# Performance work log

Measured on AMD Instinct MI355X. Metric: run time of the kernel, lower is better.

## Reference

```python
import jax, jax.numpy as jnp
import numpy as np

B, N, R = 2, 64, 16
D = 64      # node_dim_in
H = 256     # hidden_dim
EOUT = 64   # edge_dim_out
PSTEP = 2


def _lin_init(key, fi, fo):
    k1, k2 = jax.random.split(key)
    s = 1.0 / np.sqrt(fi)
    W = jax.random.uniform(k1, (fi, fo), minval=-s, maxval=s, dtype=jnp.float32)
    b = jax.random.uniform(k2, (fo,), minval=-s, maxval=s, dtype=jnp.float32)
    return W, b


def setup_inputs() -> dict:
    key = jax.random.key(0)
    ks = jax.random.split(key, 11)
    node_rep = jax.random.normal(ks[0], (B, N, R, D), dtype=jnp.float32)
    ne_W, ne_b = _lin_init(ks[1], D, H)          # node_encoder
    ee_W, ee_b = _lin_init(ks[2], 2 * D, H)      # edge_encoder (edge_rep is None)
    np_W1, np_b1 = _lin_init(ks[3], 3 * H, H)    # node_propagator
    np_W2, np_b2 = _lin_init(ks[4], H, H)
    ep0_W1, ep0_b1 = _lin_init(ks[5], 3 * H, H)  # edge_propagators[0]
    ep0_W2, ep0_b2 = _lin_init(ks[6], H, H)
    ep1_W1, ep1_b1 = _lin_init(ks[7], 3 * H, H)  # edge_propagators[1]
    ep1_W2, ep1_b2 = _lin_init(ks[8], H, H)
    pr_W1, pr_b1 = _lin_init(ks[9], 2 * H, H)    # edge_predictor
    pr_W2, pr_b2 = _lin_init(ks[10], H, EOUT)
    return dict(node_rep=node_rep, ne_W=ne_W, ne_b=ne_b, ee_W=ee_W, ee_b=ee_b,
                np_W1=np_W1, np_b1=np_b1, np_W2=np_W2, np_b2=np_b2,
                ep0_W1=ep0_W1, ep0_b1=ep0_b1, ep0_W2=ep0_W2, ep0_b2=ep0_b2,
                ep1_W1=ep1_W1, ep1_b1=ep1_b1, ep1_W2=ep1_W2, ep1_b2=ep1_b2,
                pr_W1=pr_W1, pr_b1=pr_b1, pr_W2=pr_W2, pr_b2=pr_b2)


def _propnet(node_rep, ne_W, ne_b, ee_W, ee_b, np_W1, np_b1, np_W2, np_b2,
             ep_params, pr_W1, pr_b1, pr_W2, pr_b2):
    relu = jax.nn.relu
    # node encoder: [B,N,R,H]
    node_enc = relu(node_rep @ ne_W + ne_b)
    # edge encoder on cat(node_rep_r, node_rep_s): split the weight instead of
    # materializing the [B,N,N,R,2D] repeated-concat tensor (same math).
    # receiver varies over axis 1, sender over axis 2.
    edge_enc = relu(node_rep[:, :, None] @ ee_W[:D]
                    + node_rep[:, None, :] @ ee_W[D:] + ee_b)  # [B,N,N,R,H]
    node_effect = node_enc
    edge_effect = edge_enc
    for (W1, b1, W2, b2) in ep_params:
        # edge propagator on cat(effect_r, effect_s, edge_effect)
        h = relu(node_effect[:, :, None] @ W1[:H]
                 + node_effect[:, None, :] @ W1[H:2 * H]
                 + edge_effect @ W1[2 * H:] + b1)
        edge_effect = relu(h @ W2 + b2)                 # [B,N,N,R,H]
        agg = edge_effect.sum(axis=2)                   # sum over senders -> [B,N,R,H]
        g = relu(node_enc @ np_W1[:H]
                 + node_effect @ np_W1[H:2 * H]
                 + agg @ np_W1[2 * H:] + np_b1)
        node_effect = relu(g @ np_W2 + np_b2)
    # edge predictor on cat(edge_effect, edge_enc) -> split weight
    p = relu(edge_effect @ pr_W1[:H] + edge_enc @ pr_W1[H:] + pr_b1)
    edge_pred = p @ pr_W2 + pr_b2                       # [B,N,N,R,EOUT]
    return edge_pred


def reference(node_rep, ne_W, ne_b, ee_W, ee_b, np_W1, np_b1, np_W2, np_b2,
              ep0_W1, ep0_b1, ep0_W2, ep0_b2, ep1_W1, ep1_b1, ep1_W2, ep1_b2,
              pr_W1, pr_b1, pr_W2, pr_b2):
    ep_params = [(ep0_W1, ep0_b1, ep0_W2, ep0_b2), (ep1_W1, ep1_b1, ep1_W2, ep1_b2)]
    return _propnet(node_rep, ne_W, ne_b, ee_W, ee_b, np_W1, np_b1, np_W2, np_b2,
                    ep_params, pr_W1, pr_b1, pr_W2, pr_b2)
```

## Files before the change

### kernel.cpp

```cpp
#include <hip/hip_runtime.h>
#include <hip/hip_bf16.h>


typedef __attribute__((ext_vector_type(8))) short short8;
typedef __attribute__((ext_vector_type(4))) float f32x4;
typedef __attribute__((ext_vector_type(2))) unsigned int u32x2;

#define DI __device__ __forceinline__

constexpr size_t WF_SZ = 131072;
constexpr size_t OFF_NEW  = 14 * WF_SZ;
constexpr size_t OFF_EE1  = OFF_NEW + 32768;
constexpr size_t OFF_EE2  = OFF_EE1 + 32768;
constexpr size_t OFF_PW2  = OFF_EE2 + 32768;
constexpr size_t OFF_NENC = OFF_PW2 + 32768;
constexpr size_t OFF_X1   = OFF_NENC + (size_t)2048 * 256 * 2;
constexpr size_t SM = (size_t)2048 * 256 * 4;
constexpr size_t OFF_X2  = OFF_X1 + SM;
constexpr size_t OFF_E1  = OFF_X2 + SM;
constexpr size_t OFF_E2  = OFF_E1 + SM;
constexpr size_t OFF_NE1 = OFF_E2 + SM;
constexpr size_t OFF_AGG = OFF_NE1 + SM;
constexpr size_t OFF_IMG = OFF_AGG + 2 * SM;

DI unsigned short f2bf(float f) {
    unsigned u = __builtin_bit_cast(unsigned, f);
    u += 0x7fffu + ((u >> 16) & 1u);
    return (unsigned short)(u >> 16);
}

DI int kmap(int g, int e) { return 4 * g + (e & 3) + ((e >> 2) << 4); }

DI void dma16(const void* g, void* l) {
    __builtin_amdgcn_global_load_lds((const __attribute__((address_space(1))) void*)g,
                                     (__attribute__((address_space(3))) void*)l, 16, 0, 0);
}

__global__ __launch_bounds__(64) void kconv(const float* ep0W1, const float* ep0W2,
                                            const float* ep1W1, const float* ep1W2,
                                            const float* prW1, const float* prW2,
                                            const float* npW1, const float* npW2,
                                            const float* neW, const float* eeW,
                                            unsigned short* wsu)
{
    int bid = blockIdx.x, l = threadIdx.x;
    const float* src; unsigned short* dst; int NT = 16, ld = 256, f;
    if (bid < 1792) {
        int m = bid >> 7; f = bid & 127;
        switch (m) {
            case 0:  src = ep0W1 + 512 * 256; break;
            case 1:  src = ep0W2;             break;
            case 2:  src = ep1W1 + 512 * 256; break;
            case 3:  src = ep1W2;             break;
            case 4:  src = prW1;              break;
            case 5:  src = prW1 + 256 * 256;  break;
            case 6:  src = ep0W1;             break;
            case 7:  src = ep0W1 + 256 * 256; break;
            case 8:  src = npW1 + 256 * 256;  break;
            case 9:  src = npW1 + 512 * 256;  break;
            case 10: src = npW1;              break;
            case 11: src = npW2;              break;
            case 12: src = ep1W1;             break;
            default: src = ep1W1 + 256 * 256; break;
        }
        dst = wsu + (size_t)m * (WF_SZ / 2);
    } else if (bid < 1888) {
        int m = (bid - 1792) >> 5; f = (bid - 1792) & 31;
        src = (m == 0) ? neW : (m == 1) ? eeW : eeW + 64 * 256;
        dst = wsu + ((m == 0) ? OFF_NEW : (m == 1) ? OFF_EE1 : OFF_EE2) / 2;
    } else {
        f = bid - 1888; NT = 4; ld = 64; src = prW2; dst = wsu + OFF_PW2 / 2;
    }
    int kt = f / NT, nt = f % NT;
    int g = l >> 4, c = nt * 16 + (l & 15);
    unsigned short* o = dst + (size_t)((kt * NT + nt) * 64 + l) * 8;
#pragma unroll
    for (int e = 0; e < 8; ++e) {
        int k = 32 * kt + kmap(g, e);
        o[e] = f2bf(src[(size_t)k * ld + c]);
    }
}

template <int LDB>
DI short8 load_afrag(const unsigned char* lds, int row, int kt, int g) {
    int sw = (row & 7) << 4;
    int kb = 64 * kt + 8 * g;
    union { short8 s; u32x2 u[2]; } u_;
    u_.u[0] = *(const u32x2*)(lds + row * LDB + (kb ^ sw));
    u_.u[1] = *(const u32x2*)(lds + row * LDB + ((kb + 32) ^ sw));
    return u_.s;
}

template <int MI>
DI void zero_acc(f32x4 (&acc)[MI][4]) {
#pragma unroll
    for (int mi = 0; mi < MI; ++mi)
#pragma unroll
        for (int ni = 0; ni < 4; ++ni) acc[mi][ni] = (f32x4){0.f, 0.f, 0.f, 0.f};
}

template <int MI, int KT, int LDB>
DI void gemm_tile(const unsigned char* lds, const unsigned short* Wf,
                  f32x4 (&acc)[MI][4], int wv, int l) {
    const int g = l >> 4, l15 = l & 15;
    for (int kt = 0; kt < KT; ++kt) {
        short8 af[MI];
#pragma unroll
        for (int mi = 0; mi < MI; ++mi) af[mi] = load_afrag<LDB>(lds, 16 * mi + l15, kt, g);
        short8 bf[4];
#pragma unroll
        for (int ni = 0; ni < 4; ++ni)
            bf[ni] = *(const short8*)(Wf + (size_t)((kt * 16 + 4 * wv + ni) * 64 + l) * 8);
#pragma unroll
        for (int ni = 0; ni < 4; ++ni)
#pragma unroll
            for (int mi = 0; mi < MI; ++mi)
                acc[mi][ni] = __builtin_amdgcn_mfma_f32_16x16x32_bf16(af[mi], bf[ni], acc[mi][ni], 0, 0, 0);
    }
}

DI void store_tile_f32(float* dst, int r0, f32x4 (&acc)[4][4], int wv, int l) {
    int g = l >> 4, l15 = l & 15;
#pragma unroll
    for (int ni = 0; ni < 4; ++ni) {
        int col = 64 * wv + 16 * ni + l15;
#pragma unroll
        for (int mi = 0; mi < 4; ++mi)
#pragma unroll
            for (int q = 0; q < 4; ++q)
                dst[(size_t)(r0 + 16 * mi + 4 * g + q) * 256 + col] = acc[mi][ni][q];
    }
}

__global__ __launch_bounds__(256) void knode12(const float* node_rep, const float* neb,
        const unsigned short* neWf, const unsigned short* eeW1f, const unsigned short* eeW2f,
        const unsigned short* E1wf, const unsigned short* E2wf, const unsigned short* NE1wf,
        unsigned short* node_enc, float* X1, float* X2, float* E1, float* E2, float* NE1)
{
    __shared__ __align__(16) unsigned char ldsA[64 * 128];
    __shared__ __align__(16) unsigned char ldsB[64 * 512];
    const int r0 = blockIdx.x * 64, tid = threadIdx.x;
    {
        int row = tid >> 2, c0 = (tid & 3) * 16;
        const float* src = node_rep + (size_t)(r0 + row) * 64 + c0;
        union { short8 s; unsigned short u[8]; } v0, v1;
#pragma unroll
        for (int e = 0; e < 8; ++e) { v0.u[e] = f2bf(src[e]); v1.u[e] = f2bf(src[8 + e]); }
        int sw = (row & 7) << 4;
        *(short8*)&ldsA[row * 128 + ((c0 * 2) ^ sw)] = v0.s;
        *(short8*)&ldsA[row * 128 + ((c0 * 2 + 16) ^ sw)] = v1.s;
    }
    __syncthreads();
    const int l = tid & 63, wv = tid >> 6, g = l >> 4, l15 = l & 15;
    f32x4 acc[4][4];
    zero_acc(acc);
    gemm_tile<4, 2, 128>(ldsA, neWf, acc, wv, l);
#pragma unroll
    for (int ni = 0; ni < 4; ++ni) {
        int col = 64 * wv + 16 * ni + l15;
        float bb = neb[col];
#pragma unroll
        for (int mi = 0; mi < 4; ++mi)
#pragma unroll
            for (int q = 0; q < 4; ++q) {
                int row = 16 * mi + 4 * g + q;
                unsigned short bv = f2bf(fmaxf(acc[mi][ni][q] + bb, 0.f));
                *(unsigned short*)&ldsB[row * 512 + ((col * 2) ^ ((row & 7) << 4))] = bv;
                node_enc[(size_t)(r0 + row) * 256 + col] = bv;
            }
    }
    zero_acc(acc);
    gemm_tile<4, 2, 128>(ldsA, eeW1f, acc, wv, l);
    store_tile_f32(X1, r0, acc, wv, l);
    zero_acc(acc);
    gemm_tile<4, 2, 128>(ldsA, eeW2f, acc, wv, l);
    store_tile_f32(X2, r0, acc, wv, l);
    __syncthreads();
    zero_acc(acc);
    gemm_tile<4, 8, 512>(ldsB, E1wf, acc, wv, l);
    store_tile_f32(E1, r0, acc, wv, l);
    zero_acc(acc);
    gemm_tile<4, 8, 512>(ldsB, E2wf, acc, wv, l);
    store_tile_f32(E2, r0, acc, wv, l);
    zero_acc(acc);
    gemm_tile<4, 8, 512>(ldsB, NE1wf, acc, wv, l);
    store_tile_f32(NE1, r0, acc, wv, l);
}

__global__ __launch_bounds__(256) void knode3(const unsigned short* node_enc, const float* agg,
        const float* NE1, const float* npb1, const float* npb2,
        const unsigned short* NE2wf, const unsigned short* NAGGwf, const unsigned short* npW2f,
        const unsigned short* ep1Awf, const unsigned short* ep1Bwf,
        float* E1, float* E2)
{
    __shared__ __align__(16) unsigned char ldsA[64 * 512];
    __shared__ __align__(16) unsigned char ldsB[64 * 512];
    const int r0 = blockIdx.x * 64, tid = threadIdx.x;
    {
        int row = tid >> 2, cbase = (tid & 3) * 64;
        int sw = (row & 7) << 4;
#pragma unroll
        for (int cc = 0; cc < 4; ++cc) {
            int c0 = cbase + cc * 16;
            short8 lo = *(const short8*)(node_enc + (size_t)(r0 + row) * 256 + c0);
            short8 hi = *(const short8*)(node_enc + (size_t)(r0 + row) * 256 + c0 + 8);
            *(short8*)&ldsA[row * 512 + ((c0 * 2) ^ sw)] = lo;
            *(short8*)&ldsA[row * 512 + ((c0 * 2 + 16) ^ sw)] = hi;
            union { short8 s; unsigned short u[8]; } v0, v1;
            const float* aA = agg + (size_t)(r0 + row) * 256 + c0;
            const float* aB = aA + (size_t)2048 * 256;
#pragma unroll
            for (int e = 0; e < 8; ++e) {
                v0.u[e] = f2bf(aA[e] + aB[e]);
                v1.u[e] = f2bf(aA[8 + e] + aB[8 + e]);
            }
            *(short8*)&ldsB[row * 512 + ((c0 * 2) ^ sw)] = v0.s;
            *(short8*)&ldsB[row * 512 + ((c0 * 2 + 16) ^ sw)] = v1.s;
        }
    }
    __syncthreads();
    const int l = tid & 63, wv = tid >> 6, g = l >> 4, l15 = l & 15;
    f32x4 acc[4][4];
    zero_acc(acc);
    gemm_tile<4, 8, 512>(ldsA, NE2wf, acc, wv, l);
    gemm_tile<4, 8, 512>(ldsB, NAGGwf, acc, wv, l);
    __syncthreads();
#pragma unroll
    for (int ni = 0; ni < 4; ++ni) {
        int col = 64 * wv + 16 * ni + l15;
        float bb = npb1[col];
#pragma unroll
        for (int mi = 0; mi < 4; ++mi)
#pragma unroll
            for (int q = 0; q < 4; ++q) {
                int row = 16 * mi + 4 * g + q;
                float v = fmaxf(acc[mi][ni][q] + NE1[(size_t)(r0 + row) * 256 + col] + bb, 0.f);
                *(unsigned short*)&ldsA[row * 512 + ((col * 2) ^ ((row & 7) << 4))] = f2bf(v);
            }
    }
    __syncthreads();
    zero_acc(acc);
    gemm_tile<4, 8, 512>(ldsA, npW2f, acc, wv, l);
    __syncthreads();
#pragma unroll
    for (int ni = 0; ni < 4; ++ni) {
        int col = 64 * wv + 16 * ni + l15;
        float bb = npb2[col];
#pragma unroll
        for (int mi = 0; mi < 4; ++mi)
#pragma unroll
            for (int q = 0; q < 4; ++q) {
                int row = 16 * mi + 4 * g + q;
                *(unsigned short*)&ldsB[row * 512 + ((col * 2) ^ ((row & 7) << 4))] =
                    f2bf(fmaxf(acc[mi][ni][q] + bb, 0.f));
            }
    }
    __syncthreads();
    zero_acc(acc);
    gemm_tile<4, 8, 512>(ldsB, ep1Awf, acc, wv, l);
    store_tile_f32(E1, r0, acc, wv, l);
    zero_acc(acc);
    gemm_tile<4, 8, 512>(ldsB, ep1Bwf, acc, wv, l);
    store_tile_f32(E2, r0, acc, wv, l);
}

__global__ __launch_bounds__(256, 2) void kstep1(const float* X1, const float* X2, const float* eeb,
                                                 const float* E1, const float* E2,
                                                 const float* b1, const float* b2,
                                                 const unsigned short* WfA, const unsigned short* WfB,
                                                 unsigned char* img, float* agg)
{
    __shared__ __align__(16) unsigned char T[32 * 512];
    const int bb = blockIdx.x, tid = threadIdx.x;
    const int bir = bb >> 1, half = bb & 1;
    const int b = bir >> 10, r = bir & 15;

    {
        int rlo = tid >> 5;
        int c0 = (tid & 31) * 8;
        for (int p = 0; p < 4; ++p) {
            int row = p * 8 + rlo;
            union { short8 s; unsigned short u[8]; } v;
            int nrj = b * 1024 + (half * 32 + row) * 16 + r;
#pragma unroll
            for (int e = 0; e < 8; ++e) {
                float x = X1[(size_t)bir * 256 + c0 + e] + X2[(size_t)nrj * 256 + c0 + e] + eeb[c0 + e];
                v.u[e] = f2bf(fmaxf(x, 0.f));
            }
            *(short8*)&T[row * 512 + ((c0 * 2) ^ ((row & 7) << 4))] = v.s;
        }
    }
    __syncthreads();

    const int l = tid & 63, wv = tid >> 6, g = l >> 4, l15 = l & 15;
    f32x4 acc[2][4];
    zero_acc(acc);
    gemm_tile<2, 8, 512>(T, WfA, acc, wv, l);
    __syncthreads();
#pragma unroll
    for (int ni = 0; ni < 4; ++ni) {
        int col = 64 * wv + 16 * ni + l15;
        float e1b = E1[(size_t)bir * 256 + col] + b1[col];
#pragma unroll
        for (int mi = 0; mi < 2; ++mi)
#pragma unroll
            for (int q = 0; q < 4; ++q) {
                int row = 16 * mi + 4 * g + q;
                float e2 = E2[(size_t)(b * 1024 + (half * 32 + row) * 16 + r) * 256 + col];
                float h = fmaxf(acc[mi][ni][q] + e1b + e2, 0.f);
                *(unsigned short*)&T[row * 512 + ((col * 2) ^ ((row & 7) << 4))] = f2bf(h);
                acc[mi][ni][q] = 0.f;
            }
    }
    __syncthreads();
    gemm_tile<2, 8, 512>(T, WfB, acc, wv, l);
    unsigned short* out16 = (unsigned short*)(img + (size_t)bb * 16384);
#pragma unroll
    for (int ni = 0; ni < 4; ++ni) {
        int col = 64 * wv + 16 * ni + l15;
        float bb2 = b2[col];
        float s = 0.f;
#pragma unroll
        for (int mi = 0; mi < 2; ++mi)
#pragma unroll
            for (int q = 0; q < 4; ++q) {
                int row = 16 * mi + 4 * g + q;
                float e = fmaxf(acc[mi][ni][q] + bb2, 0.f);
                out16[(row * 512 + ((col * 2) ^ ((row & 7) << 4))) >> 1] = f2bf(e);
                s += e;
            }
        s += __shfl_xor(s, 16);
        s += __shfl_xor(s, 32);
        if (l < 16) agg[((size_t)half * 2048 + bir) * 256 + 64 * wv + 16 * ni + l] = s;
    }
}

__global__ __launch_bounds__(256, 2) void kstep2pred(const float* X1, const float* X2, const float* eeb,
        const float* E1, const float* E2, const float* b1, const float* b2,
        const unsigned short* WfA, const unsigned short* WfB,
        const unsigned short* WfPA, const unsigned short* WfPB, const unsigned short* WfP2,
        const float* prb1, const float* prb2,
        const unsigned char* img, float* out)
{
    __shared__ __align__(16) unsigned char T[32 * 512];
    const int bb = blockIdx.x, tid = threadIdx.x;
    const int bir = bb >> 1, half = bb & 1;
    const int b = bir >> 10, r = bir & 15;
    const int ebase = (bir >> 4) * 1024 + r;
    const int l = tid & 63, wv = tid >> 6, g = l >> 4, l15 = l & 15;

    {
        const unsigned char* src = img + (size_t)bb * 16384;
#pragma unroll
        for (int p = 0; p < 4; ++p) {
            int chunk = wv * 4 + p;
            dma16(src + chunk * 1024 + l * 16, &T[chunk * 1024]);
        }
    }
    __syncthreads();

    f32x4 acc[2][4];
    zero_acc(acc);
    gemm_tile<2, 8, 512>(T, WfA, acc, wv, l);
    __syncthreads();
#pragma unroll
    for (int ni = 0; ni < 4; ++ni) {
        int col = 64 * wv + 16 * ni + l15;
        float e1b = E1[(size_t)bir * 256 + col] + b1[col];
#pragma unroll
        for (int mi = 0; mi < 2; ++mi)
#pragma unroll
            for (int q = 0; q < 4; ++q) {
                int row = 16 * mi + 4 * g + q;
                float e2 = E2[(size_t)(b * 1024 + (half * 32 + row) * 16 + r) * 256 + col];
                float h = fmaxf(acc[mi][ni][q] + e1b + e2, 0.f);
                *(unsigned short*)&T[row * 512 + ((col * 2) ^ ((row & 7) << 4))] = f2bf(h);
                acc[mi][ni][q] = 0.f;
            }
    }
    __syncthreads();
    gemm_tile<2, 8, 512>(T, WfB, acc, wv, l);
    __syncthreads();
#pragma unroll
    for (int ni = 0; ni < 4; ++ni) {
        int col = 64 * wv + 16 * ni + l15;
        float bb2 = b2[col];
#pragma unroll
        for (int mi = 0; mi < 2; ++mi)
#pragma unroll
            for (int q = 0; q < 4; ++q) {
                int row = 16 * mi + 4 * g + q;
                *(unsigned short*)&T[row * 512 + ((col * 2) ^ ((row & 7) << 4))] =
                    f2bf(fmaxf(acc[mi][ni][q] + bb2, 0.f));
            }
    }
    __syncthreads();
    zero_acc(acc);
    gemm_tile<2, 8, 512>(T, WfPA, acc, wv, l);
    __syncthreads();
    {
        int rlo = tid >> 5;
        int c0 = (tid & 31) * 8;
        for (int p = 0; p < 4; ++p) {
            int row = p * 8 + rlo;
            union { short8 s; unsigned short u[8]; } v;
            int nrj = b * 1024 + (half * 32 + row) * 16 + r;
#pragma unroll
            for (int e = 0; e < 8; ++e) {
                float x = X1[(size_t)bir * 256 + c0 + e] + X2[(size_t)nrj * 256 + c0 + e] + eeb[c0 + e];
                v.u[e] = f2bf(fmaxf(x, 0.f));
            }
            *(short8*)&T[row * 512 + ((c0 * 2) ^ ((row & 7) << 4))] = v.s;
        }
    }
    __syncthreads();
    gemm_tile<2, 8, 512>(T, WfPB, acc, wv, l);
    __syncthreads();
#pragma unroll
    for (int ni = 0; ni < 4; ++ni) {
        int col = 64 * wv + 16 * ni + l15;
        float pb = prb1[col];
#pragma unroll
        for (int mi = 0; mi < 2; ++mi)
#pragma unroll
            for (int q = 0; q < 4; ++q) {
                int row = 16 * mi + 4 * g + q;
                float p = fmaxf(acc[mi][ni][q] + pb, 0.f);
                *(unsigned short*)&T[row * 512 + ((col * 2) ^ ((row & 7) << 4))] = f2bf(p);
            }
    }
    __syncthreads();
    f32x4 acc3[2];
#pragma unroll
    for (int mi = 0; mi < 2; ++mi) acc3[mi] = (f32x4){0.f, 0.f, 0.f, 0.f};
    for (int kt = 0; kt < 8; ++kt) {
        short8 bf = *(const short8*)(WfP2 + (size_t)((kt * 4 + wv) * 64 + l) * 8);
#pragma unroll
        for (int mi = 0; mi < 2; ++mi) {
            short8 af = load_afrag<512>(T, 16 * mi + l15, kt, g);
            acc3[mi] = __builtin_amdgcn_mfma_f32_16x16x32_bf16(af, bf, acc3[mi], 0, 0, 0);
        }
    }
    int colo = 16 * wv + l15;
    float pb2 = prb2[colo];
#pragma unroll
    for (int mi = 0; mi < 2; ++mi)
#pragma unroll
        for (int q = 0; q < 4; ++q) {
            int row = 16 * mi + 4 * g + q;
            out[(size_t)(ebase + (half * 32 + row) * 16) * 64 + colo] = acc3[mi][q] + pb2;
        }
}

extern "C" void kernel_launch(void* const* d_in, const int* in_sizes, int n_in,
                              void* d_out, int out_size, void* d_ws, size_t ws_size,
                              hipStream_t stream)
{
    (void)in_sizes; (void)n_in; (void)out_size; (void)ws_size;
    const float* node_rep = (const float*)d_in[0];
    const float* neW   = (const float*)d_in[1];
    const float* neb   = (const float*)d_in[2];
    const float* eeW   = (const float*)d_in[3];
    const float* eeb   = (const float*)d_in[4];
    const float* npW1  = (const float*)d_in[5];
    const float* npb1  = (const float*)d_in[6];
    const float* npW2  = (const float*)d_in[7];
    const float* npb2  = (const float*)d_in[8];
    const float* ep0W1 = (const float*)d_in[9];
    const float* ep0b1 = (const float*)d_in[10];
    const float* ep0W2 = (const float*)d_in[11];
    const float* ep0b2 = (const float*)d_in[12];
    const float* ep1W1 = (const float*)d_in[13];
    const float* ep1b1 = (const float*)d_in[14];
    const float* ep1W2 = (const float*)d_in[15];
    const float* ep1b2 = (const float*)d_in[16];
    const float* prW1  = (const float*)d_in[17];
    const float* prb1  = (const float*)d_in[18];
    const float* prW2  = (const float*)d_in[19];
    const float* prb2  = (const float*)d_in[20];

    char* ws = (char*)d_ws;
    unsigned short* wsu = (unsigned short*)ws;
    auto wfull = [&](int i) { return (const unsigned short*)(ws + (size_t)i * WF_SZ); };
    unsigned short* node_enc = (unsigned short*)(ws + OFF_NENC);
    float* X1  = (float*)(ws + OFF_X1);
    float* X2  = (float*)(ws + OFF_X2);
    float* E1  = (float*)(ws + OFF_E1);
    float* E2  = (float*)(ws + OFF_E2);
    float* NE1 = (float*)(ws + OFF_NE1);
    float* agg = (float*)(ws + OFF_AGG);
    unsigned char* img = (unsigned char*)(ws + OFF_IMG);
    const unsigned short* neWf  = (const unsigned short*)(ws + OFF_NEW);
    const unsigned short* eeW1f = (const unsigned short*)(ws + OFF_EE1);
    const unsigned short* eeW2f = (const unsigned short*)(ws + OFF_EE2);
    const unsigned short* prW2f = (const unsigned short*)(ws + OFF_PW2);

    kconv<<<dim3(1920), dim3(64), 0, stream>>>(ep0W1, ep0W2, ep1W1, ep1W2, prW1, prW2,
                                               npW1, npW2, neW, eeW, wsu);
    knode12<<<dim3(32), dim3(256), 0, stream>>>(node_rep, neb, neWf, eeW1f, eeW2f,
                                                wfull(6), wfull(7), wfull(10),
                                                node_enc, X1, X2, E1, E2, NE1);
    kstep1<<<dim3(4096), dim3(256), 0, stream>>>(X1, X2, eeb, E1, E2, ep0b1, ep0b2,
                                                 wfull(0), wfull(1), img, agg);
    knode3<<<dim3(32), dim3(256), 0, stream>>>(node_enc, agg, NE1, npb1, npb2,
                                               wfull(8), wfull(9), wfull(11),
                                               wfull(12), wfull(13), E1, E2);
    kstep2pred<<<dim3(4096), dim3(256), 0, stream>>>(X1, X2, eeb, E1, E2, ep1b1, ep1b2,
                                                     wfull(2), wfull(3), wfull(4), wfull(5),
                                                     prW2f, prb1, prb2, img, (float*)d_out);
}
```

Measured before the change: 381.8 us.

## Store sender projection as swizzled bf16 image, DMA into LDS in edge kernels

The per-sender E2 projection is now written by the node kernels as a bf16, pre-swizzled per (batch, relation) image that the edge kernels copy into a new LDS buffer with async global-to-LDS loads. This replaces strided fp32 global gathers in the epilogue. The E1 bias is folded in when E1 is stored. The node kernels also move to 32-row tiles so they launch twice as many blocks. The cost is an extra 16 KB of LDS per edge block, which may reduce occupancy, and bf16 rounding of E2.

```diff
diff --git a/kernel.cpp b/kernel.cpp
--- a/kernel.cpp
+++ b/kernel.cpp
@@ -16,17 +16,21 @@
 constexpr size_t OFF_NENC = OFF_PW2 + 32768;
 constexpr size_t OFF_X1   = OFF_NENC + (size_t)2048 * 256 * 2;
 constexpr size_t SM = (size_t)2048 * 256 * 4;
-constexpr size_t OFF_X2  = OFF_X1 + SM;
-constexpr size_t OFF_E1  = OFF_X2 + SM;
-constexpr size_t OFF_E2  = OFF_E1 + SM;
-constexpr size_t OFF_NE1 = OFF_E2 + SM;
-constexpr size_t OFF_AGG = OFF_NE1 + SM;
-constexpr size_t OFF_IMG = OFF_AGG + 2 * SM;
+constexpr size_t OFF_X2   = OFF_X1 + SM;
+constexpr size_t OFF_E1   = OFF_X2 + SM;
+constexpr size_t OFF_E2I  = OFF_E1 + SM;
+constexpr size_t OFF_NE1  = OFF_E2I + 32 * 32768;
+constexpr size_t OFF_AGG  = OFF_NE1 + SM;
+constexpr size_t OFF_IMG  = OFF_AGG + 2 * SM;
 
 DI unsigned short f2bf(float f) {
     unsigned u = __builtin_bit_cast(unsigned, f);
     u += 0x7fffu + ((u >> 16) & 1u);
     return (unsigned short)(u >> 16);
+}
+DI float bf2f(unsigned short s) {
+    unsigned u = (unsigned)s << 16;
+    return __builtin_bit_cast(float, u);
 }
 
 DI int kmap(int g, int e) { return 4 * g + (e & 3) + ((e >> 2) << 4); }
@@ -119,48 +123,81 @@
     }
 }
 
-DI void store_tile_f32(float* dst, int r0, f32x4 (&acc)[4][4], int wv, int l) {
+template <int MI>
+DI void store_tile_f32(float* dst, int r0, f32x4 (&acc)[MI][4], int wv, int l) {
     int g = l >> 4, l15 = l & 15;
 #pragma unroll
     for (int ni = 0; ni < 4; ++ni) {
         int col = 64 * wv + 16 * ni + l15;
 #pragma unroll
-        for (int mi = 0; mi < 4; ++mi)
+        for (int mi = 0; mi < MI; ++mi)
 #pragma unroll
             for (int q = 0; q < 4; ++q)
                 dst[(size_t)(r0 + 16 * mi + 4 * g + q) * 256 + col] = acc[mi][ni][q];
     }
 }
 
+template <int MI>
+DI void store_tile_bias(float* dst, const float* bias, int r0, f32x4 (&acc)[MI][4], int wv, int l) {
+    int g = l >> 4, l15 = l & 15;
+#pragma unroll
+    for (int ni = 0; ni < 4; ++ni) {
+        int col = 64 * wv + 16 * ni + l15;
+        float bb = bias[col];
+#pragma unroll
+        for (int mi = 0; mi < MI; ++mi)
+#pragma unroll
+            for (int q = 0; q < 4; ++q)
+                dst[(size_t)(r0 + 16 * mi + 4 * g + q) * 256 + col] = acc[mi][ni][q] + bb;
+    }
+}
+
+template <int MI>
+DI void store_E2img(unsigned char* E2img, int r0, f32x4 (&acc)[MI][4], int wv, int l) {
+    int g = l >> 4, l15 = l & 15;
+#pragma unroll
+    for (int ni = 0; ni < 4; ++ni) {
+        int col = 64 * wv + 16 * ni + l15;
+#pragma unroll
+        for (int mi = 0; mi < MI; ++mi)
+#pragma unroll
+            for (int q = 0; q < 4; ++q) {
+                int nr = r0 + 16 * mi + 4 * g + q;
+                int b = nr >> 10, j = (nr >> 4) & 63, r = nr & 15;
+                size_t byte = (size_t)(b * 16 + r) * 32768 + ((j * 512 + col * 2) ^ ((j & 7) << 4));
+                *(unsigned short*)(E2img + byte) = f2bf(acc[mi][ni][q]);
+            }
+    }
+}
+
 __global__ __launch_bounds__(256) void knode12(const float* node_rep, const float* neb,
+        const float* ep0b1,
         const unsigned short* neWf, const unsigned short* eeW1f, const unsigned short* eeW2f,
         const unsigned short* E1wf, const unsigned short* E2wf, const unsigned short* NE1wf,
-        unsigned short* node_enc, float* X1, float* X2, float* E1, float* E2, float* NE1)
+        unsigned short* node_enc, float* X1, float* X2, float* E1b, unsigned char* E2img, float* NE1)
 {
-    __shared__ __align__(16) unsigned char ldsA[64 * 128];
-    __shared__ __align__(16) unsigned char ldsB[64 * 512];
-    const int r0 = blockIdx.x * 64, tid = threadIdx.x;
+    __shared__ __align__(16) unsigned char ldsA[32 * 128];
+    __shared__ __align__(16) unsigned char ldsB[32 * 512];
+    const int r0 = blockIdx.x * 32, tid = threadIdx.x;
     {
-        int row = tid >> 2, c0 = (tid & 3) * 16;
+        int row = tid >> 3, c0 = (tid & 7) * 8;
         const float* src = node_rep + (size_t)(r0 + row) * 64 + c0;
-        union { short8 s; unsigned short u[8]; } v0, v1;
-#pragma unroll
-        for (int e = 0; e < 8; ++e) { v0.u[e] = f2bf(src[e]); v1.u[e] = f2bf(src[8 + e]); }
-        int sw = (row & 7) << 4;
-        *(short8*)&ldsA[row * 128 + ((c0 * 2) ^ sw)] = v0.s;
-        *(short8*)&ldsA[row * 128 + ((c0 * 2 + 16) ^ sw)] = v1.s;
+        union { short8 s; unsigned short u[8]; } v;
+#pragma unroll
+        for (int e = 0; e < 8; ++e) v.u[e] = f2bf(src[e]);
+        *(short8*)&ldsA[row * 128 + ((c0 * 2) ^ ((row & 7) << 4))] = v.s;
     }
     __syncthreads();
     const int l = tid & 63, wv = tid >> 6, g = l >> 4, l15 = l & 15;
-    f32x4 acc[4][4];
-    zero_acc(acc);
-    gemm_tile<4, 2, 128>(ldsA, neWf, acc, wv, l);
+    f32x4 acc[2][4];
+    zero_acc(acc);
+    gemm_tile<2, 2, 128>(ldsA, neWf, acc, wv, l);
 #pragma unroll
     for (int ni = 0; ni < 4; ++ni) {
         int col = 64 * wv + 16 * ni + l15;
         float bb = neb[col];
 #pragma unroll
-        for (int mi = 0; mi < 4; ++mi)
+        for (int mi = 0; mi < 2; ++mi)
 #pragma unroll
             for (int q = 0; q < 4; ++q) {
                 int row = 16 * mi + 4 * g + q;
@@ -170,37 +207,37 @@
             }
     }
     zero_acc(acc);
-    gemm_tile<4, 2, 128>(ldsA, eeW1f, acc, wv, l);
-    store_tile_f32(X1, r0, acc, wv, l);
-    zero_acc(acc);
-    gemm_tile<4, 2, 128>(ldsA, eeW2f, acc, wv, l);
-    store_tile_f32(X2, r0, acc, wv, l);
-    __syncthreads();
-    zero_acc(acc);
-    gemm_tile<4, 8, 512>(ldsB, E1wf, acc, wv, l);
-    store_tile_f32(E1, r0, acc, wv, l);
-    zero_acc(acc);
-    gemm_tile<4, 8, 512>(ldsB, E2wf, acc, wv, l);
-    store_tile_f32(E2, r0, acc, wv, l);
-    zero_acc(acc);
-    gemm_tile<4, 8, 512>(ldsB, NE1wf, acc, wv, l);
-    store_tile_f32(NE1, r0, acc, wv, l);
+    gemm_tile<2, 2, 128>(ldsA, eeW1f, acc, wv, l);
+    store_tile_f32<2>(X1, r0, acc, wv, l);
+    zero_acc(acc);
+    gemm_tile<2, 2, 128>(ldsA, eeW2f, acc, wv, l);
+    store_tile_f32<2>(X2, r0, acc, wv, l);
+    __syncthreads();
+    zero_acc(acc);
+    gemm_tile<2, 8, 512>(ldsB, E1wf, acc, wv, l);
+    store_tile_bias<2>(E1b, ep0b1, r0, acc, wv, l);
+    zero_acc(acc);
+    gemm_tile<2, 8, 512>(ldsB, E2wf, acc, wv, l);
+    store_E2img<2>(E2img, r0, acc, wv, l);
+    zero_acc(acc);
+    gemm_tile<2, 8, 512>(ldsB, NE1wf, acc, wv, l);
+    store_tile_f32<2>(NE1, r0, acc, wv, l);
 }
 
 __global__ __launch_bounds__(256) void knode3(const unsigned short* node_enc, const float* agg,
-        const float* NE1, const float* npb1, const float* npb2,
+        const float* NE1, const float* npb1, const float* npb2, const float* ep1b1,
         const unsigned short* NE2wf, const unsigned short* NAGGwf, const unsigned short* npW2f,
         const unsigned short* ep1Awf, const unsigned short* ep1Bwf,
-        float* E1, float* E2)
+        float* E1b, unsigned char* E2img)
 {
-    __shared__ __align__(16) unsigned char ldsA[64 * 512];
-    __shared__ __align__(16) unsigned char ldsB[64 * 512];
-    const int r0 = blockIdx.x * 64, tid = threadIdx.x;
+    __shared__ __align__(16) unsigned char ldsA[32 * 512];
+    __shared__ __align__(16) unsigned char ldsB[32 * 512];
+    const int r0 = blockIdx.x * 32, tid = threadIdx.x;
     {
-        int row = tid >> 2, cbase = (tid & 3) * 64;
+        int row = tid >> 3, cbase = (tid & 7) * 32;
         int sw = (row & 7) << 4;
 #pragma unroll
-        for (int cc = 0; cc < 4; ++cc) {
+        for (int cc = 0; cc < 2; ++cc) {
             int c0 = cbase + cc * 16;
             short8 lo = *(const short8*)(node_enc + (size_t)(r0 + row) * 256 + c0);
             short8 hi = *(const short8*)(node_enc + (size_t)(r0 + row) * 256 + c0 + 8);
@@ -220,17 +257,17 @@
     }
     __syncthreads();
     const int l = tid & 63, wv = tid >> 6, g = l >> 4, l15 = l & 15;
-    f32x4 acc[4][4];
-    zero_acc(acc);
-    gemm_tile<4, 8, 512>(ldsA, NE2wf, acc, wv, l);
-    gemm_tile<4, 8, 512>(ldsB, NAGGwf, acc, wv, l);
+    f32x4 acc[2][4];
+    zero_acc(acc);
+    gemm_tile<2, 8, 512>(ldsA, NE2wf, acc, wv, l);
+    gemm_tile<2, 8, 512>(ldsB, NAGGwf, acc, wv, l);
     __syncthreads();
 #pragma unroll
     for (int ni = 0; ni < 4; ++ni) {
         int col = 64 * wv + 16 * ni + l15;
         float bb = npb1[col];
 #pragma unroll
-        for (int mi = 0; mi < 4; ++mi)
+        for (int mi = 0; mi < 2; ++mi)
 #pragma unroll
             for (int q = 0; q < 4; ++q) {
                 int row = 16 * mi + 4 * g + q;
@@ -240,14 +277,14 @@
     }
     __syncthreads();
     zero_acc(acc);
-    gemm_tile<4, 8, 512>(ldsA, npW2f, acc, wv, l);
+    gemm_tile<2, 8, 512>(ldsA, npW2f, acc, wv, l);
     __syncthreads();
 #pragma unroll
     for (int ni = 0; ni < 4; ++ni) {
         int col = 64 * wv + 16 * ni + l15;
         float bb = npb2[col];
 #pragma unroll
-        for (int mi = 0; mi < 4; ++mi)
+        for (int mi = 0; mi < 2; ++mi)
 #pragma unroll
             for (int q = 0; q < 4; ++q) {
                 int row = 16 * mi + 4 * g + q;
@@ -257,24 +294,34 @@
     }
     __syncthreads();
     zero_acc(acc);
-    gemm_tile<4, 8, 512>(ldsB, ep1Awf, acc, wv, l);
-    store_tile_f32(E1, r0, acc, wv, l);
-    zero_acc(acc);
-    gemm_tile<4, 8, 512>(ldsB, ep1Bwf, acc, wv, l);
-    store_tile_f32(E2, r0, acc, wv, l);
+    gemm_tile<2, 8, 512>(ldsB, ep1Awf, acc, wv, l);
+    store_tile_bias<2>(E1b, ep1b1, r0, acc, wv, l);
+    zero_acc(acc);
+    gemm_tile<2, 8, 512>(ldsB, ep1Bwf, acc, wv, l);
+    store_E2img<2>(E2img, r0, acc, wv, l);
 }
 
 __global__ __launch_bounds__(256, 2) void kstep1(const float* X1, const float* X2, const float* eeb,
-                                                 const float* E1, const float* E2,
-                                                 const float* b1, const float* b2,
+                                                 const float* E1b, const unsigned char* E2img,
+                                                 const float* b2,
                                                  const unsigned short* WfA, const unsigned short* WfB,
                                                  unsigned char* img, float* agg)
 {
     __shared__ __align__(16) unsigned char T[32 * 512];
+    __shared__ __align__(16) unsigned char L2e[32 * 512];
     const int bb = blockIdx.x, tid = threadIdx.x;
     const int bir = bb >> 1, half = bb & 1;
     const int b = bir >> 10, r = bir & 15;
-
+    const int l = tid & 63, wv = tid >> 6, g = l >> 4, l15 = l & 15;
+
+    {
+        const unsigned char* src = E2img + (size_t)(b * 16 + r) * 32768 + (size_t)half * 16384;
+#pragma unroll
+        for (int p = 0; p < 4; ++p) {
+            int chunk = wv * 4 + p;
+            dma16(src + chunk * 1024 + l * 16, &L2e[chunk * 1024]);
+        }
+    }
     {
         int rlo = tid >> 5;
         int c0 = (tid & 31) * 8;
@@ -292,7 +339,6 @@
     }
     __syncthreads();
 
-    const int l = tid & 63, wv = tid >> 6, g = l >> 4, l15 = l & 15;
     f32x4 acc[2][4];
     zero_acc(acc);
     gemm_tile<2, 8, 512>(T, WfA, acc, wv, l);
@@ -300,13 +346,13 @@
 #pragma unroll
     for (int ni = 0; ni < 4; ++ni) {
         int col = 64 * wv + 16 * ni + l15;
-        float e1b = E1[(size_t)bir * 256 + col] + b1[col];
-#pragma unroll
-        for (int mi = 0; mi < 2; ++mi)
-#pragma unroll
-            for (int q = 0; q < 4; ++q) {
-                int row = 16 * mi + 4 * g + q;
-                float e2 = E2[(size_t)(b * 1024 + (half * 32 + row) * 16 + r) * 256 + col];
+        float e1b = E1b[(size_t)bir * 256 + col];
+#pragma unroll
+        for (int mi = 0; mi < 2; ++mi)
+#pragma unroll
+            for (int q = 0; q < 4; ++q) {
+                int row = 16 * mi + 4 * g + q;
+                float e2 = bf2f(*(const unsigned short*)&L2e[row * 512 + ((col * 2) ^ ((row & 7) << 4))]);
                 float h = fmaxf(acc[mi][ni][q] + e1b + e2, 0.f);
                 *(unsigned short*)&T[row * 512 + ((col * 2) ^ ((row & 7) << 4))] = f2bf(h);
                 acc[mi][ni][q] = 0.f;
@@ -336,13 +382,14 @@
 }
 
 __global__ __launch_bounds__(256, 2) void kstep2pred(const float* X1, const float* X2, const float* eeb,
-        const float* E1, const float* E2, const float* b1, const float* b2,
+        const float* E1b, const unsigned char* E2img, const float* b2,
         const unsigned short* WfA, const unsigned short* WfB,
         const unsigned short* WfPA, const unsigned short* WfPB, const unsigned short* WfP2,
         const float* prb1, const float* prb2,
         const unsigned char* img, float* out)
 {
     __shared__ __align__(16) unsigned char T[32 * 512];
+    __shared__ __align__(16) unsigned char L2e[32 * 512];
     const int bb = blockIdx.x, tid = threadIdx.x;
     const int bir = bb >> 1, half = bb & 1;
     const int b = bir >> 10, r = bir & 15;
@@ -351,10 +398,12 @@
 
     {
         const unsigned char* src = img + (size_t)bb * 16384;
+        const unsigned char* srcE = E2img + (size_t)(b * 16 + r) * 32768 + (size_t)half * 16384;
 #pragma unroll
         for (int p = 0; p < 4; ++p) {
             int chunk = wv * 4 + p;
             dma16(src + chunk * 1024 + l * 16, &T[chunk * 1024]);
+            dma16(srcE + chunk * 1024 + l * 16, &L2e[chunk * 1024]);
         }
     }
     __syncthreads();
@@ -366,13 +415,13 @@
 #pragma unroll
     for (int ni = 0; ni < 4; ++ni) {
         int col = 64 * wv + 16 * ni + l15;
-        float e1b = E1[(size_t)bir * 256 + col] + b1[col];
-#pragma unroll
-        for (int mi = 0; mi < 2; ++mi)
-#pragma unroll
-            for (int q = 0; q < 4; ++q) {
-                int row = 16 * mi + 4 * g + q;
-                float e2 = E2[(size_t)(b * 1024 + (half * 32 + row) * 16 + r) * 256 + col];
+        float e1b = E1b[(size_t)bir * 256 + col];
+#pragma unroll
+        for (int mi = 0; mi < 2; ++mi)
+#pragma unroll
+            for (int q = 0; q < 4; ++q) {
+                int row = 16 * mi + 4 * g + q;
+                float e2 = bf2f(*(const unsigned short*)&L2e[row * 512 + ((col * 2) ^ ((row & 7) << 4))]);
                 float h = fmaxf(acc[mi][ni][q] + e1b + e2, 0.f);
                 *(unsigned short*)&T[row * 512 + ((col * 2) ^ ((row & 7) << 4))] = f2bf(h);
                 acc[mi][ni][q] = 0.f;
@@ -483,12 +532,12 @@
     unsigned short* wsu = (unsigned short*)ws;
     auto wfull = [&](int i) { return (const unsigned short*)(ws + (size_t)i * WF_SZ); };
     unsigned short* node_enc = (unsigned short*)(ws + OFF_NENC);
-    float* X1  = (float*)(ws + OFF_X1);
-    float* X2  = (float*)(ws + OFF_X2);
-    float* E1  = (float*)(ws + OFF_E1);
-    float* E2  = (float*)(ws + OFF_E2);
-    float* NE1 = (float*)(ws + OFF_NE1);
-    float* agg = (float*)(ws + OFF_AGG);
+    float* X1   = (float*)(ws + OFF_X1);
+    float* X2   = (float*)(ws + OFF_X2);
+    float* E1b  = (float*)(ws + OFF_E1);
+    unsigned char* E2img = (unsigned char*)(ws + OFF_E2I);
+    float* NE1  = (float*)(ws + OFF_NE1);
+    float* agg  = (float*)(ws + OFF_AGG);
     unsigned char* img = (unsigned char*)(ws + OFF_IMG);
     const unsigned short* neWf  = (const unsigned short*)(ws + OFF_NEW);
     const unsigned short* eeW1f = (const unsigned short*)(ws + OFF_EE1);
@@ -497,15 +546,15 @@
 
     kconv<<<dim3(1920), dim3(64), 0, stream>>>(ep0W1, ep0W2, ep1W1, ep1W2, prW1, prW2,
                                                npW1, npW2, neW, eeW, wsu);
-    knode12<<<dim3(32), dim3(256), 0, stream>>>(node_rep, neb, neWf, eeW1f, eeW2f,
+    knode12<<<dim3(64), dim3(256), 0, stream>>>(node_rep, neb, ep0b1, neWf, eeW1f, eeW2f,
                                                 wfull(6), wfull(7), wfull(10),
-                                                node_enc, X1, X2, E1, E2, NE1);
-    kstep1<<<dim3(4096), dim3(256), 0, stream>>>(X1, X2, eeb, E1, E2, ep0b1, ep0b2,
+                                                node_enc, X1, X2, E1b, E2img, NE1);
+    kstep1<<<dim3(4096), dim3(256), 0, stream>>>(X1, X2, eeb, E1b, E2img, ep0b2,
                                                  wfull(0), wfull(1), img, agg);
-    knode3<<<dim3(32), dim3(256), 0, stream>>>(node_enc, agg, NE1, npb1, npb2,
+    knode3<<<dim3(64), dim3(256), 0, stream>>>(node_enc, agg, NE1, npb1, npb2, ep1b1,
                                                wfull(8), wfull(9), wfull(11),
-                                               wfull(12), wfull(13), E1, E2);
-    kstep2pred<<<dim3(4096), dim3(256), 0, stream>>>(X1, X2, eeb, E1, E2, ep1b1, ep1b2,
+                                               wfull(12), wfull(13), E1b, E2img);
+    kstep2pred<<<dim3(4096), dim3(256), 0, stream>>>(X1, X2, eeb, E1b, E2img, ep1b2,
                                                      wfull(2), wfull(3), wfull(4), wfull(5),
                                                      prW2f, prb1, prb2, img, (float*)d_out);
 }
```

New measurement: 344.5 us. 9.8% less time.
